# Optimization experiments

Hardware: AMD Instinct MI355X
Metric: run time of the kernel (lower is better)

Reference implementation:

```python
import jax, jax.numpy as jnp
import numpy as np

N_NODES = 100000
N_EDGES = 3200000
N_GRAPHS = 64
IN_FEATS = 128
NUM_CLASSES = 10


def setup_inputs() -> dict:
    key = jax.random.key(0)
    ks = jax.random.split(key, 12)
    in_feat = jax.random.normal(ks[0], (N_NODES, IN_FEATS), dtype=jnp.float32)
    src = jax.random.randint(ks[1], (N_EDGES,), 0, N_NODES, dtype=jnp.int32)
    dst = jax.random.randint(ks[2], (N_EDGES,), 0, N_NODES, dtype=jnp.int32)
    graph_ids = jnp.sort(jax.random.randint(ks[3], (N_NODES,), 0, N_GRAPHS, dtype=jnp.int32))
    def glorot(k, fan_in, fan_out):
        s = jnp.sqrt(6.0 / (fan_in + fan_out))
        return jax.random.uniform(k, (fan_in, fan_out), jnp.float32, -s, s)
    W1 = glorot(ks[4], IN_FEATS, 64); b1 = jnp.zeros((64,), jnp.float32)
    W2 = glorot(ks[5], 64, 128);      b2 = jnp.zeros((128,), jnp.float32)
    W3 = glorot(ks[6], 128, 64);      b3 = jnp.zeros((64,), jnp.float32)
    Wd = glorot(ks[7], 64, NUM_CLASSES)
    bd = jnp.zeros((NUM_CLASSES,), jnp.float32)
    return {"in_feat": in_feat, "src": src, "dst": dst, "graph_ids": graph_ids,
            "W1": W1, "b1": b1, "W2": W2, "b2": b2, "W3": W3, "b3": b3,
            "Wd": Wd, "bd": bd}


def _graph_conv(h, src, dst, norm_src, norm_dst, W, b):
    # DGL GraphConv, norm='both': h' = D_in^{-1/2} A (D_out^{-1/2} h) W + b
    x = h * norm_src[:, None]
    m = jax.ops.segment_sum(x[src], dst, num_segments=N_NODES)
    m = m * norm_dst[:, None]
    return m @ W + b


def reference(in_feat, src, dst, graph_ids, W1, b1, W2, b2, W3, b3, Wd, bd):
    ones = jnp.ones((N_EDGES,), jnp.float32)
    deg_out = jax.ops.segment_sum(ones, src, num_segments=N_NODES)
    deg_in = jax.ops.segment_sum(ones, dst, num_segments=N_NODES)
    norm_src = jax.lax.rsqrt(jnp.clip(deg_out, 1.0))
    norm_dst = jax.lax.rsqrt(jnp.clip(deg_in, 1.0))

    h = jax.nn.relu(_graph_conv(in_feat, src, dst, norm_src, norm_dst, W1, b1))
    h = jax.nn.relu(_graph_conv(h, src, dst, norm_src, norm_dst, W2, b2))
    h = jax.nn.relu(_graph_conv(h, src, dst, norm_src, norm_dst, W3, b3))

    hg = jax.ops.segment_sum(h, graph_ids, num_segments=N_GRAPHS)  # [G, 64]
    hg = jnp.tanh(hg)
    return hg @ Wd + bd  # [G, num_classes]
```

## Files before the change

kernel.cpp:

```cpp
#include <hip/hip_runtime.h>
#include <hip/hip_bf16.h>


constexpr int NN = 100000;
constexpr int NE = 3200000;
constexpr int NG = 64;

constexpr int CBITS = 15;
constexpr int CHUNK = 1 << CBITS;
constexpr int NCHUNK = (NE + CHUNK - 1) / CHUNK;
constexpr int WORDS = NN / 4;
constexpr int HWORDS = WORDS / 2;

typedef __attribute__((ext_vector_type(8))) short short8;
typedef __attribute__((ext_vector_type(4))) float f32x4;
typedef __attribute__((ext_vector_type(2))) float f32x2;


__global__ __launch_bounds__(1024) void hist_kernel(
    const int* __restrict__ src, const int* __restrict__ dst,
    uint* __restrict__ pdst, uint* __restrict__ psrc,
    unsigned char* __restrict__ lrank) {
  __shared__ uint bins[HWORDS];
  for (int i = threadIdx.x; i < HWORDS; i += 1024) bins[i] = 0;
  __syncthreads();
  const int c = blockIdx.x, r = blockIdx.z;
  const int nlo = r * (NN / 2), nhi = nlo + NN / 2;
  const int wbase = r * HWORDS;
  const int start = c << CBITS;
  const int end = min(start + CHUNK, NE);
  const int* idx = (blockIdx.y == 0) ? dst : src;
  if (blockIdx.y == 0) {
    for (int i = start + threadIdx.x; i < end; i += 1024) {
      int n = idx[i];
      if (n >= nlo && n < nhi) {
        uint old = atomicAdd(&bins[(n >> 2) - wbase], 1u << ((n & 3) * 8));
        lrank[i] = (unsigned char)(old >> ((n & 3) * 8));
      }
    }
  } else {
    for (int i = start + threadIdx.x; i < end; i += 1024) {
      int n = idx[i];
      if (n >= nlo && n < nhi)
        atomicAdd(&bins[(n >> 2) - wbase], 1u << ((n & 3) * 8));
    }
  }
  __syncthreads();
  uint* pp = ((blockIdx.y == 0) ? pdst : psrc) + (size_t)c * WORDS + wbase;
  for (int i = threadIdx.x; i < HWORDS; i += 1024) pp[i] = bins[i];
}


__global__ __launch_bounds__(256) void reduce2_kernel(
    const uint* __restrict__ pdst, const uint* __restrict__ psrc,
    uint* __restrict__ P, int* __restrict__ deg_in,
    int* __restrict__ deg_out) {
  int w = blockIdx.x * 256 + threadIdx.x;
  if (w >= WORDS) return;
  uint run = 0;
  if (blockIdx.y == 0) {
#pragma unroll 7
    for (int c = 0; c < NCHUNK; ++c) {
      uint v = pdst[(size_t)c * WORDS + w];
      P[(size_t)c * WORDS + w] = run;
      run += v;
    }
    ((int4*)deg_in)[w] = make_int4(run & 0xff, (run >> 8) & 0xff,
                                   (run >> 16) & 0xff, (run >> 24) & 0xff);
  } else {
#pragma unroll 7
    for (int c = 0; c < NCHUNK; ++c) run += psrc[(size_t)c * WORDS + w];
    ((int4*)deg_out)[w] = make_int4(run & 0xff, (run >> 8) & 0xff,
                                    (run >> 16) & 0xff, (run >> 24) & 0xff);
  }
}

__global__ __launch_bounds__(256) void norm_kernel(
    const int* __restrict__ dout, const int* __restrict__ din,
    float* __restrict__ ns, float* __restrict__ nd, int n) {
  int i = blockIdx.x * 256 + threadIdx.x;
  if (i < n) {
    ns[i] = rsqrtf(fmaxf((float)dout[i], 1.0f));
    nd[i] = rsqrtf(fmaxf((float)din[i], 1.0f));
  }
}


__global__ __launch_bounds__(256) void scan1_kernel(
    const int* __restrict__ deg, int* __restrict__ row_off,
    int* __restrict__ bsums, int n) {
  __shared__ int s[256];
  int t = threadIdx.x;
  int base = blockIdx.x * 1024 + t * 4;
  int v0 = 0, v1 = 0, v2 = 0, v3 = 0;
  if (base + 0 < n) v0 = deg[base + 0];
  if (base + 1 < n) v1 = deg[base + 1];
  if (base + 2 < n) v2 = deg[base + 2];
  if (base + 3 < n) v3 = deg[base + 3];
  int sum = v0 + v1 + v2 + v3;
  s[t] = sum;
  __syncthreads();
  for (int off = 1; off < 256; off <<= 1) {
    int x = (t >= off) ? s[t - off] : 0;
    __syncthreads();
    s[t] += x;
    __syncthreads();
  }
  int excl = s[t] - sum;
  if (t == 255) bsums[blockIdx.x] = s[255];
  if (base + 0 < n) row_off[base + 0] = excl;
  if (base + 1 < n) row_off[base + 1] = excl + v0;
  if (base + 2 < n) row_off[base + 2] = excl + v0 + v1;
  if (base + 3 < n) row_off[base + 3] = excl + v0 + v1 + v2;
}

__global__ __launch_bounds__(128) void scan2_kernel(
    int* __restrict__ bsums, int nb, int* __restrict__ row_off, int n) {
  __shared__ int s[128];
  int t = threadIdx.x;
  int v = (t < nb) ? bsums[t] : 0;
  s[t] = v;
  __syncthreads();
  for (int off = 1; off < 128; off <<= 1) {
    int x = (t >= off) ? s[t - off] : 0;
    __syncthreads();
    s[t] += x;
    __syncthreads();
  }
  if (t < nb) bsums[t] = s[t] - v;
  if (t == 127) row_off[n] = s[127];
}

__global__ __launch_bounds__(256) void scan3_kernel(
    int* __restrict__ row_off, const int* __restrict__ bsums, int n) {
  int i = blockIdx.x * 256 + threadIdx.x;
  if (i < n) row_off[i] += bsums[i >> 10];
}


__global__ __launch_bounds__(256) void fill_kernel(
    const int* __restrict__ src, const int* __restrict__ dst,
    const int* __restrict__ row_off, const unsigned char* __restrict__ Pb,
    const unsigned char* __restrict__ lrank, int* __restrict__ csr, int e) {
  int i = blockIdx.x * 256 + threadIdx.x;
  if (i < e) {
    int d = dst[i];
    int c = i >> CBITS;
    int pos = row_off[d] + (int)Pb[(size_t)c * NN + d] + (int)lrank[i];
    csr[pos] = src[i];
  }
}


__device__ __forceinline__ uint pack_bf16(float a, float b) {
  uint ua = __float_as_uint(a), ub = __float_as_uint(b);
  ua = (ua + 0x7fffu + ((ua >> 16) & 1u)) >> 16;
  ub = (ub + 0x7fffu + ((ub >> 16) & 1u)) & 0xffff0000u;
  return ua | ub;
}

__device__ __forceinline__ ushort to_bf16(float a) {
  uint ua = __float_as_uint(a);
  return (ushort)((ua + 0x7fffu + ((ua >> 16) & 1u)) >> 16);
}

union U16 {
  uint4 u;
  short8 s;
};
__device__ __forceinline__ short8 as_short8(uint4 u) {
  U16 t;
  t.u = u;
  return t.s;
}

__device__ __forceinline__ f32x2 bf2(uint u) {
  f32x2 r;
  r.x = __uint_as_float(u << 16);
  r.y = __uint_as_float(u & 0xffff0000u);
  return r;
}

__device__ __forceinline__ void add8(f32x2* a, uint4 v) {
  a[0] += bf2(v.x);
  a[1] += bf2(v.y);
  a[2] += bf2(v.z);
  a[3] += bf2(v.w);
}


__global__ __launch_bounds__(256) void transw_kernel(
    const float* __restrict__ W1, const float* __restrict__ W2,
    const float* __restrict__ W3, ushort* __restrict__ Wt1,
    ushort* __restrict__ Wt2, ushort* __restrict__ Wt3) {
  int i = blockIdx.x * 256 + threadIdx.x;
  if (i < 8192) {
    int n = i >> 7, k = i & 127;
    Wt1[i] = to_bf16(W1[k * 64 + n]);
  } else if (i < 16384) {
    int j = i - 8192;
    int n = j >> 6, k = j & 63;
    Wt2[j] = to_bf16(W2[k * 128 + n]);
  } else if (i < 24576) {
    int j = i - 16384;
    int n = j >> 7, k = j & 127;
    Wt3[j] = to_bf16(W3[k * 64 + n]);
  }
}


template <int K, int N, bool AF32, bool RELU, bool BIAS, bool SCALE>
__global__ __launch_bounds__(256) void gemm_mfma_kernel(
    const void* __restrict__ Av, const ushort* __restrict__ Wt,
    const float* __restrict__ bias, const float* __restrict__ scale,
    ushort* __restrict__ C, int n) {
  int wid = threadIdx.x >> 6, lane = threadIdx.x & 63;
  int r = lane & 15, quad = lane >> 4;
  int m16 = blockIdx.x * 64 + wid * 16;
  if (m16 >= n) return;
  int mc = min(m16 + r, n - 1);
  constexpr int KS = K / 32;
  short8 a[KS];
  if (AF32) {
    const float* A = (const float*)Av;
#pragma unroll
    for (int ks = 0; ks < KS; ++ks) {
      const float4* p = (const float4*)(A + (size_t)mc * K + ks * 32 + quad * 8);
      float4 x = p[0], y = p[1];
      uint4 u;
      u.x = pack_bf16(x.x, x.y);
      u.y = pack_bf16(x.z, x.w);
      u.z = pack_bf16(y.x, y.y);
      u.w = pack_bf16(y.z, y.w);
      a[ks] = as_short8(u);
    }
  } else {
    const ushort* A = (const ushort*)Av;
#pragma unroll
    for (int ks = 0; ks < KS; ++ks)
      a[ks] = as_short8(*(const uint4*)(A + (size_t)mc * K + ks * 32 + quad * 8));
  }
#pragma unroll
  for (int nt = 0; nt < N / 16; ++nt) {
    f32x4 acc = {0.f, 0.f, 0.f, 0.f};
#pragma unroll
    for (int ks = 0; ks < KS; ++ks) {
      short8 b = as_short8(
          *(const uint4*)(Wt + (size_t)(nt * 16 + r) * K + ks * 32 + quad * 8));
      acc = __builtin_amdgcn_mfma_f32_16x16x32_bf16(a[ks], b, acc, 0, 0, 0);
    }
    float bv = 0.f;
    if (BIAS) bv = bias[nt * 16 + r];
#pragma unroll
    for (int reg = 0; reg < 4; ++reg) {
      int m = m16 + quad * 4 + reg;
      if (m < n) {
        float v = acc[reg] + bv;
        if (RELU) v = fmaxf(v, 0.f);
        if (SCALE) v *= scale[m];
        C[(size_t)m * N + nt * 16 + r] = to_bf16(v);
      }
    }
  }
}


__device__ __forceinline__ void gather2_bf16(const int* __restrict__ csr,
                                             const ushort* __restrict__ x,
                                             int rs, int rm, int re, int lane,
                                             f32x2* a0, f32x2* a1) {
  const int eg = lane >> 3;
  const int fl = lane & 7;
  for (int e0 = rs; e0 < re; e0 += 64) {
    int idx = e0 + lane;
    int sv = (idx < re) ? csr[idx] : 0;
    int cnt = re - e0;
    if (cnt > 64) cnt = 64;
    int c0 = rm - e0;
#pragma unroll
    for (int j = 0; j < 8; ++j) {
      int jb = j * 8;
      if (jb < cnt) {
        int s = __shfl(sv, jb + eg);
        uint4 v = *(const uint4*)(x + (size_t)s * 64 + fl * 8);
        if (jb + 8 > cnt) {
          uint mv = ((jb + eg) < cnt) ? 0xffffffffu : 0u;
          v.x &= mv; v.y &= mv; v.z &= mv; v.w &= mv;
        }
        if (jb + 8 <= c0) {
          add8(a0, v);
        } else if (jb >= c0) {
          add8(a1, v);
        } else {
          uint m0 = ((jb + eg) < c0) ? 0xffffffffu : 0u;
          uint4 v0;
          v0.x = v.x & m0; v0.y = v.y & m0; v0.z = v.z & m0; v0.w = v.w & m0;
          add8(a0, v0);
          v.x ^= v0.x; v.y ^= v0.y; v.z ^= v0.z; v.w ^= v0.w;
          add8(a1, v);
        }
      }
    }
  }
#pragma unroll
  for (int k = 0; k < 4; ++k) {
    a0[k].x += __shfl_xor(a0[k].x, 8);
    a0[k].x += __shfl_xor(a0[k].x, 16);
    a0[k].x += __shfl_xor(a0[k].x, 32);
    a0[k].y += __shfl_xor(a0[k].y, 8);
    a0[k].y += __shfl_xor(a0[k].y, 16);
    a0[k].y += __shfl_xor(a0[k].y, 32);
    a1[k].x += __shfl_xor(a1[k].x, 8);
    a1[k].x += __shfl_xor(a1[k].x, 16);
    a1[k].x += __shfl_xor(a1[k].x, 32);
    a1[k].y += __shfl_xor(a1[k].y, 8);
    a1[k].y += __shfl_xor(a1[k].y, 16);
    a1[k].y += __shfl_xor(a1[k].y, 32);
  }
}

#define ACC_SEL(k) ((eg == 0) ? a0[(k) >> 1][(k)&1] : a1[(k) >> 1][(k)&1])


__global__ __launch_bounds__(256) void agg1_kernel(
    const int* __restrict__ row_off, const int* __restrict__ csr,
    const ushort* __restrict__ t, const float* __restrict__ nd,
    const float* __restrict__ ns, const float* __restrict__ b,
    ushort* __restrict__ out, int n) {
  int wid = threadIdx.x >> 6, lane = threadIdx.x & 63;
  int n0 = blockIdx.x * 8 + wid * 2;
  int rs = row_off[n0], rm = row_off[n0 + 1], re = row_off[n0 + 2];
  f32x2 a0[4] = {{0, 0}, {0, 0}, {0, 0}, {0, 0}};
  f32x2 a1[4] = {{0, 0}, {0, 0}, {0, 0}, {0, 0}};
  gather2_bf16(csr, t, rs, rm, re, lane, a0, a1);
  int eg = lane >> 3, fl = lane & 7;
  if (eg < 2) {
    int node = n0 + eg;
    float ndv = nd[node], nsv = ns[node];
    const float4* bp = (const float4*)(b + fl * 8);
    float4 b0 = bp[0], b1v = bp[1];
    float o0 = fmaxf(ACC_SEL(0) * ndv + b0.x, 0.f) * nsv;
    float o1 = fmaxf(ACC_SEL(1) * ndv + b0.y, 0.f) * nsv;
    float o2 = fmaxf(ACC_SEL(2) * ndv + b0.z, 0.f) * nsv;
    float o3 = fmaxf(ACC_SEL(3) * ndv + b0.w, 0.f) * nsv;
    float o4 = fmaxf(ACC_SEL(4) * ndv + b1v.x, 0.f) * nsv;
    float o5 = fmaxf(ACC_SEL(5) * ndv + b1v.y, 0.f) * nsv;
    float o6 = fmaxf(ACC_SEL(6) * ndv + b1v.z, 0.f) * nsv;
    float o7 = fmaxf(ACC_SEL(7) * ndv + b1v.w, 0.f) * nsv;
    uint4 v;
    v.x = pack_bf16(o0, o1);
    v.y = pack_bf16(o2, o3);
    v.z = pack_bf16(o4, o5);
    v.w = pack_bf16(o6, o7);
    *(uint4*)(out + (size_t)node * 64 + fl * 8) = v;
  }
}


__global__ __launch_bounds__(256) void agg2_kernel(
    const int* __restrict__ row_off, const int* __restrict__ csr,
    const ushort* __restrict__ h1s, const float* __restrict__ nd,
    ushort* __restrict__ m2, int n) {
  int wid = threadIdx.x >> 6, lane = threadIdx.x & 63;
  int n0 = blockIdx.x * 8 + wid * 2;
  int rs = row_off[n0], rm = row_off[n0 + 1], re = row_off[n0 + 2];
  f32x2 a0[4] = {{0, 0}, {0, 0}, {0, 0}, {0, 0}};
  f32x2 a1[4] = {{0, 0}, {0, 0}, {0, 0}, {0, 0}};
  gather2_bf16(csr, h1s, rs, rm, re, lane, a0, a1);
  int eg = lane >> 3, fl = lane & 7;
  if (eg < 2) {
    int node = n0 + eg;
    float ndv = nd[node];
    uint4 v;
    v.x = pack_bf16(ACC_SEL(0) * ndv, ACC_SEL(1) * ndv);
    v.y = pack_bf16(ACC_SEL(2) * ndv, ACC_SEL(3) * ndv);
    v.z = pack_bf16(ACC_SEL(4) * ndv, ACC_SEL(5) * ndv);
    v.w = pack_bf16(ACC_SEL(6) * ndv, ACC_SEL(7) * ndv);
    *(uint4*)(m2 + (size_t)node * 64 + fl * 8) = v;
  }
}


__global__ __launch_bounds__(512) void agg3_kernel(
    const int* __restrict__ row_off, const int* __restrict__ csr,
    const ushort* __restrict__ t, const float* __restrict__ nd,
    const float* __restrict__ b, const int* __restrict__ gid,
    float* __restrict__ hg, int n) {
  __shared__ float sO[16][64];
  __shared__ int sG[16];
  __shared__ int uni;
  int wid = threadIdx.x >> 6, lane = threadIdx.x & 63;
  int n0 = blockIdx.x * 16 + wid * 2;
  int rs = row_off[n0], rm = row_off[n0 + 1], re = row_off[n0 + 2];
  f32x2 a0[4] = {{0, 0}, {0, 0}, {0, 0}, {0, 0}};
  f32x2 a1[4] = {{0, 0}, {0, 0}, {0, 0}, {0, 0}};
  gather2_bf16(csr, t, rs, rm, re, lane, a0, a1);
  int eg = lane >> 3, fl = lane & 7;
  if (eg < 2) {
    int node = n0 + eg;
    int row = wid * 2 + eg;
    float ndv = nd[node];
    const float4* bp = (const float4*)(b + fl * 8);
    float4 b0 = bp[0], b1v = bp[1];
    sO[row][fl * 8 + 0] = fmaxf(ACC_SEL(0) * ndv + b0.x, 0.f);
    sO[row][fl * 8 + 1] = fmaxf(ACC_SEL(1) * ndv + b0.y, 0.f);
    sO[row][fl * 8 + 2] = fmaxf(ACC_SEL(2) * ndv + b0.z, 0.f);
    sO[row][fl * 8 + 3] = fmaxf(ACC_SEL(3) * ndv + b0.w, 0.f);
    sO[row][fl * 8 + 4] = fmaxf(ACC_SEL(4) * ndv + b1v.x, 0.f);
    sO[row][fl * 8 + 5] = fmaxf(ACC_SEL(5) * ndv + b1v.y, 0.f);
    sO[row][fl * 8 + 6] = fmaxf(ACC_SEL(6) * ndv + b1v.z, 0.f);
    sO[row][fl * 8 + 7] = fmaxf(ACC_SEL(7) * ndv + b1v.w, 0.f);
  }
  if (lane == 0) sG[wid * 2] = gid[n0];
  if (lane == 8) sG[wid * 2 + 1] = gid[n0 + 1];
  __syncthreads();
  if (threadIdx.x == 0) {
    int g0 = sG[0], u = 1;
#pragma unroll
    for (int i = 1; i < 16; ++i) u &= (sG[i] == g0);
    uni = u;
  }
  __syncthreads();
  if (uni) {
    int r = threadIdx.x >> 6;
#pragma unroll
    for (int s = 8; s >= 1; s >>= 1) {
      if (r < s) sO[r][lane] += sO[r + s][lane];
      __syncthreads();
    }
    if (threadIdx.x < 64) atomicAdd(&hg[sG[0] * 64 + lane], sO[0][lane]);
  } else {
    atomicAdd(&hg[sG[wid * 2] * 64 + lane], sO[wid * 2][lane]);
    atomicAdd(&hg[sG[wid * 2 + 1] * 64 + lane], sO[wid * 2 + 1][lane]);
  }
}


__global__ __launch_bounds__(640) void readout_kernel(
    const float* __restrict__ hg, const float* __restrict__ Wd,
    const float* __restrict__ bd, float* __restrict__ out) {
  int t = threadIdx.x;
  int g = t / 10, c = t % 10;
  float o = bd[c];
#pragma unroll 8
  for (int k = 0; k < 64; ++k) o += tanhf(hg[g * 64 + k]) * Wd[k * 10 + c];
  out[t] = o;
}


extern "C" void kernel_launch(void* const* d_in, const int* in_sizes, int n_in,
                              void* d_out, int out_size, void* d_ws, size_t ws_size,
                              hipStream_t stream) {
  const float* in_feat = (const float*)d_in[0];
  const int* src = (const int*)d_in[1];
  const int* dst = (const int*)d_in[2];
  const int* gid = (const int*)d_in[3];
  const float* W1 = (const float*)d_in[4];
  const float* b1 = (const float*)d_in[5];
  const float* W2 = (const float*)d_in[6];
  const float* b2 = (const float*)d_in[7];
  const float* W3 = (const float*)d_in[8];
  const float* b3 = (const float*)d_in[9];
  const float* Wd = (const float*)d_in[10];
  const float* bd = (const float*)d_in[11];
  float* out = (float*)d_out;

  char* ws = (char*)d_ws;
  size_t o = 0;
  auto alloc = [&](size_t bytes) -> char* {
    char* p = ws + o;
    o = (o + bytes + 1023) & ~(size_t)1023;
    return p;
  };
  float* hg = (float*)alloc(NG * 64 * 4);
  size_t zero_bytes = o;
  int* deg_out = (int*)alloc(NN * 4);
  int* deg_in = (int*)alloc(NN * 4);
  float* norm_src = (float*)alloc(NN * 4);
  float* norm_dst = (float*)alloc(NN * 4);
  int* row_off = (int*)alloc((NN + 1) * 4);
  int* bsums = (int*)alloc(512);
  ushort* Wt1 = (ushort*)alloc(64 * 128 * 2);
  ushort* Wt2 = (ushort*)alloc(128 * 64 * 2);
  ushort* Wt3 = (ushort*)alloc(64 * 128 * 2);
  int* csr = (int*)alloc((size_t)NE * 4);
  ushort* tbuf = (ushort*)alloc((size_t)NN * 64 * 2);
  ushort* h1s = (ushort*)alloc((size_t)NN * 64 * 2);
  ushort* m2 = (ushort*)alloc((size_t)NN * 64 * 2);
  ushort* h2s = (ushort*)alloc((size_t)NN * 128 * 2);
  (void)ws_size;

  char* ov = (char*)m2;
  uint* pdst = (uint*)ov;
  uint* psrc = (uint*)(ov + 9800000);
  uint* Pw = (uint*)(ov + 19600000);
  unsigned char* lrank = (unsigned char*)(ov + 29400000);

  hipMemsetAsync(d_ws, 0, zero_bytes, stream);

  const int egrid = (NE + 255) / 256;
  const int ngrid = (NN + 255) / 256;
  const int sgrid = (NN + 1023) / 1024;
  const int wgrid2 = NN / 8;
  const int rgrid = (WORDS + 255) / 256;
  const int ggrid = (NN + 63) / 64;

  transw_kernel<<<96, 256, 0, stream>>>(W1, W2, W3, Wt1, Wt2, Wt3);
  hist_kernel<<<dim3(NCHUNK, 2, 2), 1024, 0, stream>>>(src, dst, pdst, psrc, lrank);
  reduce2_kernel<<<dim3(rgrid, 2), 256, 0, stream>>>(pdst, psrc, Pw, deg_in,
                                                     deg_out);
  norm_kernel<<<ngrid, 256, 0, stream>>>(deg_out, deg_in, norm_src, norm_dst, NN);
  scan1_kernel<<<sgrid, 256, 0, stream>>>(deg_in, row_off, bsums, NN);
  scan2_kernel<<<1, 128, 0, stream>>>(bsums, sgrid, row_off, NN);
  scan3_kernel<<<ngrid, 256, 0, stream>>>(row_off, bsums, NN);
  fill_kernel<<<egrid, 256, 0, stream>>>(src, dst, row_off,
                                         (const unsigned char*)Pw, lrank, csr, NE);

  gemm_mfma_kernel<128, 64, true, false, false, true>
      <<<ggrid, 256, 0, stream>>>(in_feat, Wt1, nullptr, norm_src, tbuf, NN);
  agg1_kernel<<<wgrid2, 256, 0, stream>>>(row_off, csr, tbuf, norm_dst,
                                          norm_src, b1, h1s, NN);
  agg2_kernel<<<wgrid2, 256, 0, stream>>>(row_off, csr, h1s, norm_dst, m2, NN);
  gemm_mfma_kernel<64, 128, false, true, true, true>
      <<<ggrid, 256, 0, stream>>>(m2, Wt2, b2, norm_src, h2s, NN);
  gemm_mfma_kernel<128, 64, false, false, false, false>
      <<<ggrid, 256, 0, stream>>>(h2s, Wt3, nullptr, nullptr, tbuf, NN);
  agg3_kernel<<<NN / 16, 512, 0, stream>>>(row_off, csr, tbuf, norm_dst, b3,
                                           gid, hg, NN);
  readout_kernel<<<1, 640, 0, stream>>>(hg, Wd, bd, out);
}
```

Baseline: 472.2 us.

## Pack degree histogram into 4-bit bins and fuse norm and GEMM2/GEMM3

The histogram now packs eight node counters per 32-bit LDS word, so the whole node range fits in one block's shared memory. The chunk size is doubled and the node-range split across blocks is removed. Computing the norm_src/norm_dst rsqrt is folded into the reduce kernel, which also emits byte-wide per-chunk prefixes. The layer-2 and layer-3 GEMMs are fused through an LDS tile, so the 128-wide h2s intermediate is never written to or read from global memory. The main risk is that 4-bit counters overflow into neighbouring nodes if any node receives 16 or more edges within one chunk. The pass also adds LDS traffic and register pressure in the fused GEMM.

Result: faster. 457.1 us (-3.2%).

```diff
diff --git a/kernel.cpp b/kernel.cpp
--- a/kernel.cpp
+++ b/kernel.cpp
@@ -6,11 +6,10 @@
 constexpr int NE = 3200000;
 constexpr int NG = 64;
 
-constexpr int CBITS = 15;
+constexpr int CBITS = 16;
 constexpr int CHUNK = 1 << CBITS;
 constexpr int NCHUNK = (NE + CHUNK - 1) / CHUNK;
-constexpr int WORDS = NN / 4;
-constexpr int HWORDS = WORDS / 2;
+constexpr int WORDS4 = NN / 8;
 
 typedef __attribute__((ext_vector_type(8))) short short8;
 typedef __attribute__((ext_vector_type(4))) float f32x4;
@@ -21,67 +20,80 @@
     const int* __restrict__ src, const int* __restrict__ dst,
     uint* __restrict__ pdst, uint* __restrict__ psrc,
     unsigned char* __restrict__ lrank) {
-  __shared__ uint bins[HWORDS];
-  for (int i = threadIdx.x; i < HWORDS; i += 1024) bins[i] = 0;
+  __shared__ uint bins[WORDS4];
+  for (int i = threadIdx.x; i < WORDS4; i += 1024) bins[i] = 0;
   __syncthreads();
-  const int c = blockIdx.x, r = blockIdx.z;
-  const int nlo = r * (NN / 2), nhi = nlo + NN / 2;
-  const int wbase = r * HWORDS;
+  const int c = blockIdx.x;
   const int start = c << CBITS;
   const int end = min(start + CHUNK, NE);
-  const int* idx = (blockIdx.y == 0) ? dst : src;
   if (blockIdx.y == 0) {
     for (int i = start + threadIdx.x; i < end; i += 1024) {
-      int n = idx[i];
-      if (n >= nlo && n < nhi) {
-        uint old = atomicAdd(&bins[(n >> 2) - wbase], 1u << ((n & 3) * 8));
-        lrank[i] = (unsigned char)(old >> ((n & 3) * 8));
-      }
+      int n = dst[i];
+      uint old = atomicAdd(&bins[n >> 3], 1u << ((n & 7) * 4));
+      lrank[i] = (unsigned char)((old >> ((n & 7) * 4)) & 0xf);
     }
   } else {
     for (int i = start + threadIdx.x; i < end; i += 1024) {
-      int n = idx[i];
-      if (n >= nlo && n < nhi)
-        atomicAdd(&bins[(n >> 2) - wbase], 1u << ((n & 3) * 8));
+      int n = src[i];
+      atomicAdd(&bins[n >> 3], 1u << ((n & 7) * 4));
     }
   }
   __syncthreads();
-  uint* pp = ((blockIdx.y == 0) ? pdst : psrc) + (size_t)c * WORDS + wbase;
-  for (int i = threadIdx.x; i < HWORDS; i += 1024) pp[i] = bins[i];
+  uint* pp = ((blockIdx.y == 0) ? pdst : psrc) + (size_t)c * WORDS4;
+  for (int i = threadIdx.x; i < WORDS4; i += 1024) pp[i] = bins[i];
 }
 
 
 __global__ __launch_bounds__(256) void reduce2_kernel(
     const uint* __restrict__ pdst, const uint* __restrict__ psrc,
-    uint* __restrict__ P, int* __restrict__ deg_in,
-    int* __restrict__ deg_out) {
+    unsigned char* __restrict__ Pb, int* __restrict__ deg_in,
+    float* __restrict__ nd, float* __restrict__ ns) {
   int w = blockIdx.x * 256 + threadIdx.x;
-  if (w >= WORDS) return;
-  uint run = 0;
+  if (w >= WORDS4) return;
+  uint run[8] = {0, 0, 0, 0, 0, 0, 0, 0};
   if (blockIdx.y == 0) {
 #pragma unroll 7
     for (int c = 0; c < NCHUNK; ++c) {
-      uint v = pdst[(size_t)c * WORDS + w];
-      P[(size_t)c * WORDS + w] = run;
-      run += v;
-    }
-    ((int4*)deg_in)[w] = make_int4(run & 0xff, (run >> 8) & 0xff,
-                                   (run >> 16) & 0xff, (run >> 24) & 0xff);
+      uint lo = run[0] | (run[1] << 8) | (run[2] << 16) | (run[3] << 24);
+      uint hi = run[4] | (run[5] << 8) | (run[6] << 16) | (run[7] << 24);
+      ((uint2*)(Pb + (size_t)c * NN))[w] = make_uint2(lo, hi);
+      uint v = pdst[(size_t)c * WORDS4 + w];
+#pragma unroll
+      for (int k = 0; k < 8; ++k) run[k] += (v >> (4 * k)) & 0xfu;
+    }
+    ((int4*)deg_in)[2 * w] =
+        make_int4(run[0], run[1], run[2], run[3]);
+    ((int4*)deg_in)[2 * w + 1] =
+        make_int4(run[4], run[5], run[6], run[7]);
+    float4 f0, f1;
+    f0.x = rsqrtf(fmaxf((float)run[0], 1.f));
+    f0.y = rsqrtf(fmaxf((float)run[1], 1.f));
+    f0.z = rsqrtf(fmaxf((float)run[2], 1.f));
+    f0.w = rsqrtf(fmaxf((float)run[3], 1.f));
+    f1.x = rsqrtf(fmaxf((float)run[4], 1.f));
+    f1.y = rsqrtf(fmaxf((float)run[5], 1.f));
+    f1.z = rsqrtf(fmaxf((float)run[6], 1.f));
+    f1.w = rsqrtf(fmaxf((float)run[7], 1.f));
+    ((float4*)nd)[2 * w] = f0;
+    ((float4*)nd)[2 * w + 1] = f1;
   } else {
 #pragma unroll 7
-    for (int c = 0; c < NCHUNK; ++c) run += psrc[(size_t)c * WORDS + w];
-    ((int4*)deg_out)[w] = make_int4(run & 0xff, (run >> 8) & 0xff,
-                                    (run >> 16) & 0xff, (run >> 24) & 0xff);
-  }
-}
-
-__global__ __launch_bounds__(256) void norm_kernel(
-    const int* __restrict__ dout, const int* __restrict__ din,
-    float* __restrict__ ns, float* __restrict__ nd, int n) {
-  int i = blockIdx.x * 256 + threadIdx.x;
-  if (i < n) {
-    ns[i] = rsqrtf(fmaxf((float)dout[i], 1.0f));
-    nd[i] = rsqrtf(fmaxf((float)din[i], 1.0f));
+    for (int c = 0; c < NCHUNK; ++c) {
+      uint v = psrc[(size_t)c * WORDS4 + w];
+#pragma unroll
+      for (int k = 0; k < 8; ++k) run[k] += (v >> (4 * k)) & 0xfu;
+    }
+    float4 f0, f1;
+    f0.x = rsqrtf(fmaxf((float)run[0], 1.f));
+    f0.y = rsqrtf(fmaxf((float)run[1], 1.f));
+    f0.z = rsqrtf(fmaxf((float)run[2], 1.f));
+    f0.w = rsqrtf(fmaxf((float)run[3], 1.f));
+    f1.x = rsqrtf(fmaxf((float)run[4], 1.f));
+    f1.y = rsqrtf(fmaxf((float)run[5], 1.f));
+    f1.z = rsqrtf(fmaxf((float)run[6], 1.f));
+    f1.w = rsqrtf(fmaxf((float)run[7], 1.f));
+    ((float4*)ns)[2 * w] = f0;
+    ((float4*)ns)[2 * w + 1] = f1;
   }
 }
 
@@ -209,57 +221,95 @@
 }
 
 
-template <int K, int N, bool AF32, bool RELU, bool BIAS, bool SCALE>
-__global__ __launch_bounds__(256) void gemm_mfma_kernel(
-    const void* __restrict__ Av, const ushort* __restrict__ Wt,
-    const float* __restrict__ bias, const float* __restrict__ scale,
-    ushort* __restrict__ C, int n) {
+__global__ __launch_bounds__(256) void gemm1_kernel(
+    const float* __restrict__ A, const ushort* __restrict__ Wt,
+    const float* __restrict__ scale, ushort* __restrict__ C, int n) {
   int wid = threadIdx.x >> 6, lane = threadIdx.x & 63;
   int r = lane & 15, quad = lane >> 4;
   int m16 = blockIdx.x * 64 + wid * 16;
   if (m16 >= n) return;
   int mc = min(m16 + r, n - 1);
-  constexpr int KS = K / 32;
-  short8 a[KS];
-  if (AF32) {
-    const float* A = (const float*)Av;
-#pragma unroll
-    for (int ks = 0; ks < KS; ++ks) {
-      const float4* p = (const float4*)(A + (size_t)mc * K + ks * 32 + quad * 8);
-      float4 x = p[0], y = p[1];
-      uint4 u;
-      u.x = pack_bf16(x.x, x.y);
-      u.y = pack_bf16(x.z, x.w);
-      u.z = pack_bf16(y.x, y.y);
-      u.w = pack_bf16(y.z, y.w);
-      a[ks] = as_short8(u);
-    }
-  } else {
-    const ushort* A = (const ushort*)Av;
-#pragma unroll
-    for (int ks = 0; ks < KS; ++ks)
-      a[ks] = as_short8(*(const uint4*)(A + (size_t)mc * K + ks * 32 + quad * 8));
-  }
-#pragma unroll
-  for (int nt = 0; nt < N / 16; ++nt) {
+  short8 a[4];
+#pragma unroll
+  for (int ks = 0; ks < 4; ++ks) {
+    const float4* p = (const float4*)(A + (size_t)mc * 128 + ks * 32 + quad * 8);
+    float4 x = p[0], y = p[1];
+    uint4 u;
+    u.x = pack_bf16(x.x, x.y);
+    u.y = pack_bf16(x.z, x.w);
+    u.z = pack_bf16(y.x, y.y);
+    u.w = pack_bf16(y.z, y.w);
+    a[ks] = as_short8(u);
+  }
+#pragma unroll
+  for (int nt = 0; nt < 4; ++nt) {
     f32x4 acc = {0.f, 0.f, 0.f, 0.f};
 #pragma unroll
-    for (int ks = 0; ks < KS; ++ks) {
+    for (int ks = 0; ks < 4; ++ks) {
       short8 b = as_short8(
-          *(const uint4*)(Wt + (size_t)(nt * 16 + r) * K + ks * 32 + quad * 8));
+          *(const uint4*)(Wt + (size_t)(nt * 16 + r) * 128 + ks * 32 + quad * 8));
       acc = __builtin_amdgcn_mfma_f32_16x16x32_bf16(a[ks], b, acc, 0, 0, 0);
     }
-    float bv = 0.f;
-    if (BIAS) bv = bias[nt * 16 + r];
 #pragma unroll
     for (int reg = 0; reg < 4; ++reg) {
       int m = m16 + quad * 4 + reg;
-      if (m < n) {
-        float v = acc[reg] + bv;
-        if (RELU) v = fmaxf(v, 0.f);
-        if (SCALE) v *= scale[m];
-        C[(size_t)m * N + nt * 16 + r] = to_bf16(v);
-      }
+      if (m < n) C[(size_t)m * 64 + nt * 16 + r] = to_bf16(acc[reg] * scale[m]);
+    }
+  }
+}
+
+
+__global__ __launch_bounds__(256) void gemm23_kernel(
+    const ushort* __restrict__ m2, const ushort* __restrict__ Wt2,
+    const float* __restrict__ b2, const float* __restrict__ ns,
+    const ushort* __restrict__ Wt3, ushort* __restrict__ t3, int n) {
+  __shared__ ushort sX[4][16][136];
+  int wid = threadIdx.x >> 6, lane = threadIdx.x & 63;
+  int r = lane & 15, quad = lane >> 4;
+  int m16 = blockIdx.x * 64 + wid * 16;
+  if (m16 >= n) return;
+  int mc = min(m16 + r, n - 1);
+  short8 a1[2];
+#pragma unroll
+  for (int ks = 0; ks < 2; ++ks)
+    a1[ks] = as_short8(*(const uint4*)(m2 + (size_t)mc * 64 + ks * 32 + quad * 8));
+  float nsv[4];
+#pragma unroll
+  for (int reg = 0; reg < 4; ++reg)
+    nsv[reg] = ns[min(m16 + quad * 4 + reg, n - 1)];
+#pragma unroll
+  for (int nt = 0; nt < 8; ++nt) {
+    f32x4 acc = {0.f, 0.f, 0.f, 0.f};
+#pragma unroll
+    for (int ks = 0; ks < 2; ++ks) {
+      short8 b = as_short8(
+          *(const uint4*)(Wt2 + (size_t)(nt * 16 + r) * 64 + ks * 32 + quad * 8));
+      acc = __builtin_amdgcn_mfma_f32_16x16x32_bf16(a1[ks], b, acc, 0, 0, 0);
+    }
+    float bv = b2[nt * 16 + r];
+#pragma unroll
+    for (int reg = 0; reg < 4; ++reg) {
+      float v = fmaxf(acc[reg] + bv, 0.f) * nsv[reg];
+      sX[wid][quad * 4 + reg][nt * 16 + r] = to_bf16(v);
+    }
+  }
+  short8 a2[4];
+#pragma unroll
+  for (int ks = 0; ks < 4; ++ks)
+    a2[ks] = as_short8(*(const uint4*)(&sX[wid][r][ks * 32 + quad * 8]));
+#pragma unroll
+  for (int nt = 0; nt < 4; ++nt) {
+    f32x4 acc = {0.f, 0.f, 0.f, 0.f};
+#pragma unroll
+    for (int ks = 0; ks < 4; ++ks) {
+      short8 b = as_short8(
+          *(const uint4*)(Wt3 + (size_t)(nt * 16 + r) * 128 + ks * 32 + quad * 8));
+      acc = __builtin_amdgcn_mfma_f32_16x16x32_bf16(a2[ks], b, acc, 0, 0, 0);
+    }
+#pragma unroll
+    for (int reg = 0; reg < 4; ++reg) {
+      int m = m16 + quad * 4 + reg;
+      if (m < n) t3[(size_t)m * 64 + nt * 16 + r] = to_bf16(acc[reg]);
     }
   }
 }
@@ -474,7 +524,6 @@
   };
   float* hg = (float*)alloc(NG * 64 * 4);
   size_t zero_bytes = o;
-  int* deg_out = (int*)alloc(NN * 4);
   int* deg_in = (int*)alloc(NN * 4);
   float* norm_src = (float*)alloc(NN * 4);
   float* norm_dst = (float*)alloc(NN * 4);
@@ -487,14 +536,13 @@
   ushort* tbuf = (ushort*)alloc((size_t)NN * 64 * 2);
   ushort* h1s = (ushort*)alloc((size_t)NN * 64 * 2);
   ushort* m2 = (ushort*)alloc((size_t)NN * 64 * 2);
-  ushort* h2s = (ushort*)alloc((size_t)NN * 128 * 2);
   (void)ws_size;
 
-  char* ov = (char*)m2;
+  char* ov = (char*)tbuf;
   uint* pdst = (uint*)ov;
-  uint* psrc = (uint*)(ov + 9800000);
-  uint* Pw = (uint*)(ov + 19600000);
-  unsigned char* lrank = (unsigned char*)(ov + 29400000);
+  uint* psrc = (uint*)(ov + 2457600);
+  unsigned char* Pb = (unsigned char*)(ov + 4915200);
+  unsigned char* lrank = (unsigned char*)(ov + 9830400);
 
   hipMemsetAsync(d_ws, 0, zero_bytes, stream);
 
@@ -502,29 +550,23 @@
   const int ngrid = (NN + 255) / 256;
   const int sgrid = (NN + 1023) / 1024;
   const int wgrid2 = NN / 8;
-  const int rgrid = (WORDS + 255) / 256;
+  const int rgrid = (WORDS4 + 255) / 256;
   const int ggrid = (NN + 63) / 64;
 
   transw_kernel<<<96, 256, 0, stream>>>(W1, W2, W3, Wt1, Wt2, Wt3);
-  hist_kernel<<<dim3(NCHUNK, 2, 2), 1024, 0, stream>>>(src, dst, pdst, psrc, lrank);
-  reduce2_kernel<<<dim3(rgrid, 2), 256, 0, stream>>>(pdst, psrc, Pw, deg_in,
-                                                     deg_out);
-  norm_kernel<<<ngrid, 256, 0, stream>>>(deg_out, deg_in, norm_src, norm_dst, NN);
+  hist_kernel<<<dim3(NCHUNK, 2), 1024, 0, stream>>>(src, dst, pdst, psrc, lrank);
+  reduce2_kernel<<<dim3(rgrid, 2), 256, 0, stream>>>(pdst, psrc, Pb, deg_in,
+                                                     norm_dst, norm_src);
   scan1_kernel<<<sgrid, 256, 0, stream>>>(deg_in, row_off, bsums, NN);
   scan2_kernel<<<1, 128, 0, stream>>>(bsums, sgrid, row_off, NN);
   scan3_kernel<<<ngrid, 256, 0, stream>>>(row_off, bsums, NN);
-  fill_kernel<<<egrid, 256, 0, stream>>>(src, dst, row_off,
-                                         (const unsigned char*)Pw, lrank, csr, NE);
-
-  gemm_mfma_kernel<128, 64, true, false, false, true>
-      <<<ggrid, 256, 0, stream>>>(in_feat, Wt1, nullptr, norm_src, tbuf, NN);
+  fill_kernel<<<egrid, 256, 0, stream>>>(src, dst, row_off, Pb, lrank, csr, NE);
+
+  gemm1_kernel<<<ggrid, 256, 0, stream>>>(in_feat, Wt1, norm_src, tbuf, NN);
   agg1_kernel<<<wgrid2, 256, 0, stream>>>(row_off, csr, tbuf, norm_dst,
                                           norm_src, b1, h1s, NN);
   agg2_kernel<<<wgrid2, 256, 0, stream>>>(row_off, csr, h1s, norm_dst, m2, NN);
-  gemm_mfma_kernel<64, 128, false, true, true, true>
-      <<<ggrid, 256, 0, stream>>>(m2, Wt2, b2, norm_src, h2s, NN);
-  gemm_mfma_kernel<128, 64, false, false, false, false>
-      <<<ggrid, 256, 0, stream>>>(h2s, Wt3, nullptr, nullptr, tbuf, NN);
+  gemm23_kernel<<<ggrid, 256, 0, stream>>>(m2, Wt2, b2, norm_src, Wt3, tbuf, NN);
   agg3_kernel<<<NN / 16, 512, 0, stream>>>(row_off, csr, tbuf, norm_dst, b3,
                                            gid, hg, NN);
   readout_kernel<<<1, 640, 0, stream>>>(hg, Wd, bd, out);
```
